# Performance work log

Measured on AMD Instinct MI355X. Metric: run time of the kernel, lower is better.

The kernel has to match this reference:

```python
import jax, jax.numpy as jnp
import numpy as np

N = 50000
D = 128
E = 800000
L = 3


def setup_inputs() -> dict:
    key = jax.random.key(0)
    ks = jax.random.split(key, 6)
    z = jax.random.normal(ks[0], (N, D), dtype=jnp.float32)
    edge_index = jax.random.randint(ks[1], (2, E), 0, N, dtype=jnp.int64)
    s1 = 1.0 / np.sqrt(2 * D)
    s2 = 1.0 / np.sqrt(D)
    # per-layer MLP params, stacked over layers: y = x @ W + b (W stored input-major)
    W1 = jax.random.uniform(ks[2], (L, 2 * D, D), jnp.float32, -s1, s1)
    b1 = jax.random.uniform(ks[3], (L, D), jnp.float32, -s1, s1)
    W2 = jax.random.uniform(ks[4], (L, D, D), jnp.float32, -s2, s2)
    b2 = jax.random.uniform(ks[5], (L, D), jnp.float32, -s2, s2)
    return {"z": z, "edge_index": edge_index, "W1": W1, "b1": b1, "W2": W2, "b2": b2}


def _edgeconv(h, src, dst, W1, b1, W2, b2):
    # message: mlp(cat[x_i, x_j]) per edge; x_i = target (dst), x_j = source (src)
    tmp = jnp.concatenate([h[dst], h[src]], axis=1)           # [E, 2D]
    m = jax.nn.relu(tmp @ W1 + b1) @ W2 + b2                  # [E, D]
    agg = jax.ops.segment_max(m, dst, num_segments=N)          # [N, D], -inf for empty
    return jnp.where(jnp.isfinite(agg), agg, 0.0)


def reference(z, edge_index, W1, b1, W2, b2):
    src = edge_index[0]
    dst = edge_index[1]
    h = z
    for l in range(L - 1):
        h = jax.nn.relu(_edgeconv(h, src, dst, W1[l], b1[l], W2[l], b2[l]))
    h = _edgeconv(h, src, dst, W1[L - 1], b1[L - 1], W2[L - 1], b2[L - 1])
    return h
```

## Files before the change

### kernel.cpp

```cpp
#include <hip/hip_runtime.h>

#define DH 128
#define NLAYER 3
typedef unsigned short ushort_t;
typedef __attribute__((ext_vector_type(8))) short bf16x8;
typedef __attribute__((ext_vector_type(4))) float f32x4;

__device__ __forceinline__ ushort_t f2bf(float a) {
    unsigned u = __float_as_uint(a);
    return (ushort_t)((u + 0x7fffu + ((u >> 16) & 1u)) >> 16);
}
__device__ __forceinline__ float bf2f(ushort_t h) {
    return __uint_as_float(((unsigned)h) << 16);
}
__device__ __forceinline__ unsigned cvtpk(float a, float b) {
    unsigned r;
    asm("v_cvt_pk_bf16_f32 %0, %1, %2" : "=v"(r) : "v"(a), "v"(b));
    return r;
}

__device__ __forceinline__ unsigned enc_f(float f) {
    unsigned u = __float_as_uint(f);
    return (u & 0x80000000u) ? ~u : (u | 0x80000000u);
}
__device__ __forceinline__ float dec_f(unsigned u) {
    unsigned b = (u & 0x80000000u) ? (u ^ 0x80000000u) : ~u;
    return __uint_as_float(b);
}
#define ENC_NEG_INF 0x007FFFFFu

__global__ void fill_u(unsigned* __restrict__ p, int n, unsigned v) {
    int i = blockIdx.x * blockDim.x + threadIdx.x;
    int stride = gridDim.x * blockDim.x;
    for (; i < n; i += stride) p[i] = v;
}

__global__ void hist_kernel(const int* __restrict__ dst, unsigned* __restrict__ cnt, int E) {
    int e = blockIdx.x * blockDim.x + threadIdx.x;
    int stride = gridDim.x * blockDim.x;
    for (; e < E; e += stride) atomicAdd(&cnt[dst[e]], 1u);
}

__global__ __launch_bounds__(1024) void scan_local(const unsigned* __restrict__ cnt,
                                                   unsigned* __restrict__ off,
                                                   unsigned* __restrict__ bsum, int n) {
    __shared__ unsigned s[1024];
    const int t = threadIdx.x;
    int idx = blockIdx.x * 1024 + t;
    unsigned v = (idx < n) ? cnt[idx] : 0u;
    s[t] = v;
    __syncthreads();
    for (int d = 1; d < 1024; d <<= 1) {
        unsigned u = (t >= d) ? s[t - d] : 0u;
        __syncthreads();
        s[t] += u;
        __syncthreads();
    }
    if (idx < n) off[idx] = s[t] - v;
    if (t == 1023) bsum[blockIdx.x] = s[t];
}
__global__ void scan_base(unsigned* __restrict__ bsum, int nb) {
    __shared__ unsigned s[64];
    const int t = threadIdx.x;
    unsigned v = (t < nb) ? bsum[t] : 0u;
    s[t] = v;
    __syncthreads();
    for (int d = 1; d < 64; d <<= 1) {
        unsigned u = (t >= d) ? s[t - d] : 0u;
        __syncthreads();
        s[t] += u;
        __syncthreads();
    }
    if (t < nb) bsum[t] = s[t] - v;
}
__global__ void scan_add(unsigned* __restrict__ off, const unsigned* __restrict__ bsum,
                         unsigned* __restrict__ cnt, int n) {
    int i = blockIdx.x * blockDim.x + threadIdx.x;
    int stride = gridDim.x * blockDim.x;
    for (; i < n; i += stride) { off[i] += bsum[i >> 10]; cnt[i] = 0u; }
}

__global__ void scatter_kernel(const int* __restrict__ src, const int* __restrict__ dst,
                               const unsigned* __restrict__ off, unsigned* __restrict__ cur,
                               int* __restrict__ s_src, int* __restrict__ s_dst, int E) {
    int e = blockIdx.x * blockDim.x + threadIdx.x;
    int stride = gridDim.x * blockDim.x;
    for (; e < E; e += stride) {
        int d = dst[e];
        unsigned p = off[d] + atomicAdd(&cur[d], 1u);
        s_src[p] = src[e];
        s_dst[p] = d;
    }
}

__global__ void convert_w(const float* __restrict__ W1, const float* __restrict__ W2,
                          ushort_t* __restrict__ W1t_hi, ushort_t* __restrict__ W1t_lo,
                          ushort_t* __restrict__ W2t_hi, ushort_t* __restrict__ W2t_lo) {
    const int T1 = NLAYER * 256 * DH, T2 = NLAYER * DH * DH;
    int i = blockIdx.x * blockDim.x + threadIdx.x;
    int stride = gridDim.x * blockDim.x;
    for (; i < T1 + T2; i += stride) {
        if (i < T1) {
            int l = i >> 15, r = i & 32767, c = r >> 7, k = r & 127;
            float w = W1[(size_t)l * 32768 + (size_t)((c < 128) ? k : 128 + k) * DH + (c & 127)];
            ushort_t hi = f2bf(w);
            W1t_hi[i] = hi; W1t_lo[i] = f2bf(w - bf2f(hi));
        } else {
            int j = i - T1;
            int l = j >> 14, r = j & 16383, c = r >> 7, k = r & 127;
            float w = W2[(size_t)l * 16384 + (size_t)k * DH + c];
            ushort_t hi = f2bf(w);
            W2t_hi[j] = hi; W2t_lo[j] = f2bf(w - bf2f(hi));
        }
    }
}

__global__ __launch_bounds__(256, 2) void node_gemm(
    const float* __restrict__ zin, const unsigned* __restrict__ aggin,
    const float* __restrict__ b2prev,
    const ushort_t* __restrict__ wthi, const ushort_t* __restrict__ wtlo,
    const float* __restrict__ b1, float* __restrict__ outA, float* __restrict__ outB,
    int N, int nrb, int mode) {
    __shared__ char smem[33280];
    float* b2s = (float*)(smem + 32768);
    const int t = threadIdx.x;
    const int w = t >> 6, l = t & 63;
    const int bb = blockIdx.x;
    const int half = (bb >= nrb) ? 1 : 0;
    const ushort_t* whi = wthi + (size_t)(half ? 128 : 0) * DH;
    const ushort_t* wlo = wtlo + (size_t)(half ? 128 : 0) * DH;
    float* outp = half ? outB : outA;
    const int n0 = (bb - half * nrb) * 128;

    if (t < 128) b2s[t] = mode ? b2prev[t] : 0.0f;
    #pragma unroll
    for (int i = 0; i < 4; ++i) {
        int cid = i * 256 + t;
        int cc = cid >> 4, ch = cid & 15;
        int sc = ch ^ (cc & 15);
        uint4 vh = *(const uint4*)(whi + (size_t)cc * DH + sc * 8);
        uint4 vl = *(const uint4*)(wlo + (size_t)cc * DH + sc * 8);
        *(uint4*)(smem + cid * 16) = vh;
        *(uint4*)(smem + 16384 + cid * 16) = vl;
    }
    __syncthreads();

    bf16x8 ahi[2][4], alo[2][4];
    #pragma unroll
    for (int rt = 0; rt < 2; ++rt) {
        int row = n0 + w * 32 + rt * 16 + (l & 15);
        if (row >= N) row = N - 1;
        size_t base = (size_t)row * DH + 8 * (l >> 4);
        const int kbase = 8 * (l >> 4);
        #pragma unroll
        for (int ks = 0; ks < 4; ++ks) {
            float v0, v1, v2, v3, v4, v5, v6, v7;
            if (mode == 0) {
                float4 a0 = *(const float4*)(zin + base + ks * 32);
                float4 a1 = *(const float4*)(zin + base + ks * 32 + 4);
                v0 = a0.x; v1 = a0.y; v2 = a0.z; v3 = a0.w;
                v4 = a1.x; v5 = a1.y; v6 = a1.z; v7 = a1.w;
            } else {
                uint4 u0 = *(const uint4*)(aggin + base + ks * 32);
                uint4 u1 = *(const uint4*)(aggin + base + ks * 32 + 4);
                float4 c0 = *(const float4*)&b2s[kbase + ks * 32];
                float4 c1 = *(const float4*)&b2s[kbase + ks * 32 + 4];
                v0 = fmaxf((u0.x == ENC_NEG_INF) ? 0.0f : dec_f(u0.x) + c0.x, 0.0f);
                v1 = fmaxf((u0.y == ENC_NEG_INF) ? 0.0f : dec_f(u0.y) + c0.y, 0.0f);
                v2 = fmaxf((u0.z == ENC_NEG_INF) ? 0.0f : dec_f(u0.z) + c0.z, 0.0f);
                v3 = fmaxf((u0.w == ENC_NEG_INF) ? 0.0f : dec_f(u0.w) + c0.w, 0.0f);
                v4 = fmaxf((u1.x == ENC_NEG_INF) ? 0.0f : dec_f(u1.x) + c1.x, 0.0f);
                v5 = fmaxf((u1.y == ENC_NEG_INF) ? 0.0f : dec_f(u1.y) + c1.y, 0.0f);
                v6 = fmaxf((u1.z == ENC_NEG_INF) ? 0.0f : dec_f(u1.z) + c1.z, 0.0f);
                v7 = fmaxf((u1.w == ENC_NEG_INF) ? 0.0f : dec_f(u1.w) + c1.w, 0.0f);
            }
            unsigned h01 = cvtpk(v0, v1), h23 = cvtpk(v2, v3);
            unsigned h45 = cvtpk(v4, v5), h67 = cvtpk(v6, v7);
            float l0 = v0 - __uint_as_float(h01 << 16);
            float l1 = v1 - __uint_as_float(h01 & 0xffff0000u);
            float l2 = v2 - __uint_as_float(h23 << 16);
            float l3 = v3 - __uint_as_float(h23 & 0xffff0000u);
            float l4 = v4 - __uint_as_float(h45 << 16);
            float l5 = v5 - __uint_as_float(h45 & 0xffff0000u);
            float l6 = v6 - __uint_as_float(h67 << 16);
            float l7 = v7 - __uint_as_float(h67 & 0xffff0000u);
            unsigned q01 = cvtpk(l0, l1), q23 = cvtpk(l2, l3);
            unsigned q45 = cvtpk(l4, l5), q67 = cvtpk(l6, l7);
            uint4 hp = {h01, h23, h45, h67};
            uint4 lp = {q01, q23, q45, q67};
            ahi[rt][ks] = *(bf16x8*)&hp;
            alo[rt][ks] = *(bf16x8*)&lp;
        }
    }
    f32x4 acc[2][8];
    #pragma unroll
    for (int rt = 0; rt < 2; ++rt)
        #pragma unroll
        for (int ct = 0; ct < 8; ++ct) acc[rt][ct] = (f32x4){0.f, 0.f, 0.f, 0.f};
    #pragma unroll
    for (int ct = 0; ct < 4; ++ct) {
        int colv = ct * 16 + (l & 15);
        #pragma unroll
        for (int ks = 0; ks < 4; ++ks) {
            int chb = ks * 4 + (l >> 4);
            int addr = colv * 256 + ((chb ^ (colv & 15)) << 4);
            bf16x8 bh = *(const bf16x8*)(smem + addr);
            bf16x8 bl = *(const bf16x8*)(smem + 16384 + addr);
            #pragma unroll
            for (int rt = 0; rt < 2; ++rt) {
                acc[rt][ct] = __builtin_amdgcn_mfma_f32_16x16x32_bf16(ahi[rt][ks], bh, acc[rt][ct], 0, 0, 0);
                acc[rt][ct] = __builtin_amdgcn_mfma_f32_16x16x32_bf16(ahi[rt][ks], bl, acc[rt][ct], 0, 0, 0);
                acc[rt][ct] = __builtin_amdgcn_mfma_f32_16x16x32_bf16(alo[rt][ks], bh, acc[rt][ct], 0, 0, 0);
            }
        }
    }
    __syncthreads();
    #pragma unroll
    for (int i = 0; i < 4; ++i) {
        int cid = i * 256 + t;
        int cc = cid >> 4, ch = cid & 15;
        int sc = ch ^ (cc & 15);
        uint4 vh = *(const uint4*)(whi + (size_t)(64 + cc) * DH + sc * 8);
        uint4 vl = *(const uint4*)(wlo + (size_t)(64 + cc) * DH + sc * 8);
        *(uint4*)(smem + cid * 16) = vh;
        *(uint4*)(smem + 16384 + cid * 16) = vl;
    }
    __syncthreads();
    #pragma unroll
    for (int ct = 4; ct < 8; ++ct) {
        int colv = ct * 16 + (l & 15);
        #pragma unroll
        for (int ks = 0; ks < 4; ++ks) {
            int chb = ks * 4 + (l >> 4);
            int addr = (colv & 63) * 256 + ((chb ^ (colv & 15)) << 4);
            bf16x8 bh = *(const bf16x8*)(smem + addr);
            bf16x8 bl = *(const bf16x8*)(smem + 16384 + addr);
            #pragma unroll
            for (int rt = 0; rt < 2; ++rt) {
                acc[rt][ct] = __builtin_amdgcn_mfma_f32_16x16x32_bf16(ahi[rt][ks], bh, acc[rt][ct], 0, 0, 0);
                acc[rt][ct] = __builtin_amdgcn_mfma_f32_16x16x32_bf16(ahi[rt][ks], bl, acc[rt][ct], 0, 0, 0);
                acc[rt][ct] = __builtin_amdgcn_mfma_f32_16x16x32_bf16(alo[rt][ks], bh, acc[rt][ct], 0, 0, 0);
            }
        }
    }
    #pragma unroll
    for (int ct = 0; ct < 8; ++ct) {
        int col = ct * 16 + (l & 15);
        float bv = half ? 0.0f : b1[col];
        #pragma unroll
        for (int rt = 0; rt < 2; ++rt)
            #pragma unroll
            for (int i = 0; i < 4; ++i) {
                int row = n0 + w * 32 + rt * 16 + (l >> 4) * 4 + i;
                if (row < N) outp[(size_t)row * DH + col] = acc[rt][ct][i] + bv;
            }
    }
}

__global__ __launch_bounds__(256, 2) void edge_mlp(
    const float* __restrict__ Afp, const float* __restrict__ Bfp,
    const int* __restrict__ src, const int* __restrict__ dst,
    const ushort_t* __restrict__ w2hi, const ushort_t* __restrict__ w2lo,
    unsigned* __restrict__ agg, int E) {
    __shared__ char smem[33280];
    int* sdst = (int*)(smem + 32768);
    float* R = (float*)smem;
    const int t = threadIdx.x;
    const int w = t >> 6, l = t & 63;
    const int e0 = blockIdx.x * 128;

    if (t < 128) sdst[t] = dst[e0 + t];
    #pragma unroll
    for (int i = 0; i < 4; ++i) {
        int cid = i * 256 + t;
        int cc = cid >> 4, ch = cid & 15;
        int sc = ch ^ (cc & 15);
        uint4 vh = *(const uint4*)(w2hi + (size_t)cc * DH + sc * 8);
        uint4 vl = *(const uint4*)(w2lo + (size_t)cc * DH + sc * 8);
        *(uint4*)(smem + cid * 16) = vh;
        *(uint4*)(smem + 16384 + cid * 16) = vl;
    }

    bf16x8 ahi[2][4], alo[2][4];
    #pragma unroll
    for (int rt = 0; rt < 2; ++rt) {
        int er = w * 32 + rt * 16 + (l & 15);
        int dn = dst[e0 + er], sn = src[e0 + er];
        const float* pa = Afp + (size_t)dn * DH + 8 * (l >> 4);
        const float* pb = Bfp + (size_t)sn * DH + 8 * (l >> 4);
        #pragma unroll
        for (int ks = 0; ks < 4; ++ks) {
            float4 a0 = *(const float4*)(pa + ks * 32);
            float4 a1 = *(const float4*)(pa + ks * 32 + 4);
            float4 b0 = *(const float4*)(pb + ks * 32);
            float4 b1 = *(const float4*)(pb + ks * 32 + 4);
            float v0 = fmaxf(a0.x + b0.x, 0.f), v1 = fmaxf(a0.y + b0.y, 0.f);
            float v2 = fmaxf(a0.z + b0.z, 0.f), v3 = fmaxf(a0.w + b0.w, 0.f);
            float v4 = fmaxf(a1.x + b1.x, 0.f), v5 = fmaxf(a1.y + b1.y, 0.f);
            float v6 = fmaxf(a1.z + b1.z, 0.f), v7 = fmaxf(a1.w + b1.w, 0.f);
            unsigned h01 = cvtpk(v0, v1), h23 = cvtpk(v2, v3);
            unsigned h45 = cvtpk(v4, v5), h67 = cvtpk(v6, v7);
            float l0 = v0 - __uint_as_float(h01 << 16);
            float l1 = v1 - __uint_as_float(h01 & 0xffff0000u);
            float l2 = v2 - __uint_as_float(h23 << 16);
            float l3 = v3 - __uint_as_float(h23 & 0xffff0000u);
            float l4 = v4 - __uint_as_float(h45 << 16);
            float l5 = v5 - __uint_as_float(h45 & 0xffff0000u);
            float l6 = v6 - __uint_as_float(h67 << 16);
            float l7 = v7 - __uint_as_float(h67 & 0xffff0000u);
            unsigned q01 = cvtpk(l0, l1), q23 = cvtpk(l2, l3);
            unsigned q45 = cvtpk(l4, l5), q67 = cvtpk(l6, l7);
            uint4 hp = {h01, h23, h45, h67};
            uint4 lp = {q01, q23, q45, q67};
            ahi[rt][ks] = *(bf16x8*)&hp;
            alo[rt][ks] = *(bf16x8*)&lp;
        }
    }
    f32x4 acc[2][8];
    #pragma unroll
    for (int rt = 0; rt < 2; ++rt)
        #pragma unroll
        for (int ct = 0; ct < 8; ++ct) acc[rt][ct] = (f32x4){0.f, 0.f, 0.f, 0.f};
    __syncthreads();
    #pragma unroll
    for (int ct = 0; ct < 4; ++ct) {
        int colv = ct * 16 + (l & 15);
        #pragma unroll
        for (int ks = 0; ks < 4; ++ks) {
            int chb = ks * 4 + (l >> 4);
            int addr = colv * 256 + ((chb ^ (colv & 15)) << 4);
            bf16x8 bh = *(const bf16x8*)(smem + addr);
            bf16x8 bl = *(const bf16x8*)(smem + 16384 + addr);
            #pragma unroll
            for (int rt = 0; rt < 2; ++rt) {
                acc[rt][ct] = __builtin_amdgcn_mfma_f32_16x16x32_bf16(ahi[rt][ks], bh, acc[rt][ct], 0, 0, 0);
                acc[rt][ct] = __builtin_amdgcn_mfma_f32_16x16x32_bf16(ahi[rt][ks], bl, acc[rt][ct], 0, 0, 0);
                acc[rt][ct] = __builtin_amdgcn_mfma_f32_16x16x32_bf16(alo[rt][ks], bh, acc[rt][ct], 0, 0, 0);
            }
        }
    }
    __syncthreads();
    #pragma unroll
    for (int i = 0; i < 4; ++i) {
        int cid = i * 256 + t;
        int cc = cid >> 4, ch = cid & 15;
        int sc = ch ^ (cc & 15);
        uint4 vh = *(const uint4*)(w2hi + (size_t)(64 + cc) * DH + sc * 8);
        uint4 vl = *(const uint4*)(w2lo + (size_t)(64 + cc) * DH + sc * 8);
        *(uint4*)(smem + cid * 16) = vh;
        *(uint4*)(smem + 16384 + cid * 16) = vl;
    }
    __syncthreads();
    #pragma unroll
    for (int ct = 4; ct < 8; ++ct) {
        int colv = ct * 16 + (l & 15);
        #pragma unroll
        for (int ks = 0; ks < 4; ++ks) {
            int chb = ks * 4 + (l >> 4);
            int addr = (colv & 63) * 256 + ((chb ^ (colv & 15)) << 4);
            bf16x8 bh = *(const bf16x8*)(smem + addr);
            bf16x8 bl = *(const bf16x8*)(smem + 16384 + addr);
            #pragma unroll
            for (int rt = 0; rt < 2; ++rt) {
                acc[rt][ct] = __builtin_amdgcn_mfma_f32_16x16x32_bf16(ahi[rt][ks], bh, acc[rt][ct], 0, 0, 0);
                acc[rt][ct] = __builtin_amdgcn_mfma_f32_16x16x32_bf16(ahi[rt][ks], bl, acc[rt][ct], 0, 0, 0);
                acc[rt][ct] = __builtin_amdgcn_mfma_f32_16x16x32_bf16(alo[rt][ks], bh, acc[rt][ct], 0, 0, 0);
            }
        }
    }
    #pragma unroll
    for (int chh = 0; chh < 2; ++chh) {
        __syncthreads();
        #pragma unroll
        for (int rt = 0; rt < 2; ++rt)
            #pragma unroll
            for (int c4 = 0; c4 < 4; ++c4) {
                int ct = chh * 4 + c4;
                int col64 = c4 * 16 + (l & 15);
                #pragma unroll
                for (int i = 0; i < 4; ++i) {
                    int row = w * 32 + rt * 16 + (l >> 4) * 4 + i;
                    R[row * 64 + (col64 ^ (((row >> 2) & 3) << 4))] = acc[rt][ct][i];
                }
            }
        __syncthreads();
        const int col = l;
        const int r0 = w * 32;
        float run = R[r0 * 64 + (col ^ (((r0 >> 2) & 3) << 4))];
        int cur = sdst[r0];
        #pragma unroll
        for (int rr = r0 + 1; rr < r0 + 32; ++rr) {
            float x = R[rr * 64 + (col ^ (((rr >> 2) & 3) << 4))];
            int dd = sdst[rr];
            if (dd != cur) {
                atomicMax(&agg[(size_t)cur * DH + chh * 64 + col], enc_f(run));
                cur = dd; run = x;
            } else {
                run = fmaxf(run, x);
            }
        }
        atomicMax(&agg[(size_t)cur * DH + chh * 64 + col], enc_f(run));
    }
}

__global__ void finalize_kernel(const unsigned* __restrict__ agg, const float* __restrict__ b2,
                                float* __restrict__ outf, int n) {
    int i = blockIdx.x * blockDim.x + threadIdx.x;
    int stride = gridDim.x * blockDim.x;
    for (; i < n; i += stride) {
        unsigned uv = agg[i];
        outf[i] = (uv == ENC_NEG_INF) ? 0.0f : dec_f(uv) + b2[i & (DH - 1)];
    }
}

extern "C" void kernel_launch(void* const* d_in, const int* in_sizes, int n_in,
                              void* d_out, int out_size, void* d_ws, size_t ws_size,
                              hipStream_t stream) {
    const float* z  = (const float*)d_in[0];
    const int*   ei = (const int*)d_in[1];
    const float* W1 = (const float*)d_in[2];
    const float* b1 = (const float*)d_in[3];
    const float* W2 = (const float*)d_in[4];
    const float* b2 = (const float*)d_in[5];
    const int N = 50000, D = DH, E = 800000;
    const int* srcp = ei;
    const int* dstp = ei + E;

    float* Abuf = (float*)d_ws;
    float* Bbuf = Abuf + (size_t)N * D;
    unsigned* agg = (unsigned*)(Bbuf + (size_t)N * D);
    ushort_t* W1t_hi = (ushort_t*)(agg + (size_t)N * D);
    ushort_t* W1t_lo = W1t_hi + NLAYER * 256 * D;
    ushort_t* W2t_hi = W1t_lo + NLAYER * 256 * D;
    ushort_t* W2t_lo = W2t_hi + NLAYER * D * D;
    unsigned* cnt = (unsigned*)(W2t_lo + NLAYER * D * D);
    unsigned* off = cnt + N;
    unsigned* bsum = off + N;
    int* s_src = (int*)(bsum + 64);
    int* s_dst = s_src + E;
    float* outp = (float*)d_out;

    convert_w<<<128, 256, 0, stream>>>(W1, W2, W1t_hi, W1t_lo, W2t_hi, W2t_lo);

    const int NB = (N + 1023) / 1024;
    fill_u<<<256, 256, 0, stream>>>(cnt, N, 0u);
    hist_kernel<<<1024, 256, 0, stream>>>(dstp, cnt, E);
    scan_local<<<NB, 1024, 0, stream>>>(cnt, off, bsum, N);
    scan_base<<<1, 64, 0, stream>>>(bsum, NB);
    scan_add<<<256, 256, 0, stream>>>(off, bsum, cnt, N);
    scatter_kernel<<<1024, 256, 0, stream>>>(srcp, dstp, off, cnt, s_src, s_dst, E);

    const int nrb = (N + 127) / 128;
    for (int l = 0; l < NLAYER; ++l) {
        node_gemm<<<2 * nrb, 256, 0, stream>>>(z, agg,
                                               (l > 0) ? (b2 + (size_t)(l - 1) * D) : nullptr,
                                               W1t_hi + ((size_t)l * 256) * D,
                                               W1t_lo + ((size_t)l * 256) * D,
                                               b1 + (size_t)l * D, Abuf, Bbuf,
                                               N, nrb, (l > 0) ? 1 : 0);
        fill_u<<<2048, 256, 0, stream>>>(agg, N * D, ENC_NEG_INF);
        edge_mlp<<<E / 128, 256, 0, stream>>>(Abuf, Bbuf, s_src, s_dst,
                                              W2t_hi + (size_t)l * D * D,
                                              W2t_lo + (size_t)l * D * D, agg, E);
    }
    finalize_kernel<<<2048, 256, 0, stream>>>(agg, b2 + (size_t)2 * D, outp, N * D);
}
```

Measured before the change: 753.2 us.

## Split edge MLP output columns across 8 waves with full W2 in LDS

The edge_mlp block grows from 256 to 512 threads. Each of the 8 waves now handles 32 edges by 64 output columns instead of 32 edges by all 128 columns. The whole W2 hi/lo split is staged into 64KB of LDS once, which removes the second weight load and its extra barriers. Per-wave LDS slabs replace the shared reduction buffer for the segmented max. The cost is that each edge's A/B gather and bf16 split conversion now run in two waves, and the larger LDS footprint may limit blocks per CU.

```diff
diff --git a/kernel.cpp b/kernel.cpp
--- a/kernel.cpp
+++ b/kernel.cpp
@@ -257,34 +257,35 @@
     }
 }
 
-__global__ __launch_bounds__(256, 2) void edge_mlp(
+__global__ __launch_bounds__(512, 4) void edge_mlp(
     const float* __restrict__ Afp, const float* __restrict__ Bfp,
     const int* __restrict__ src, const int* __restrict__ dst,
     const ushort_t* __restrict__ w2hi, const ushort_t* __restrict__ w2lo,
     unsigned* __restrict__ agg, int E) {
-    __shared__ char smem[33280];
-    int* sdst = (int*)(smem + 32768);
-    float* R = (float*)smem;
+    __shared__ char smem[66048];
+    int* sdst = (int*)(smem + 65536);
     const int t = threadIdx.x;
     const int w = t >> 6, l = t & 63;
     const int e0 = blockIdx.x * 128;
+    const int ew = (w & 3) * 32;
+    const int colbase = (w >> 2) * 64;
 
     if (t < 128) sdst[t] = dst[e0 + t];
     #pragma unroll
     for (int i = 0; i < 4; ++i) {
-        int cid = i * 256 + t;
+        int cid = i * 512 + t;
         int cc = cid >> 4, ch = cid & 15;
         int sc = ch ^ (cc & 15);
         uint4 vh = *(const uint4*)(w2hi + (size_t)cc * DH + sc * 8);
         uint4 vl = *(const uint4*)(w2lo + (size_t)cc * DH + sc * 8);
         *(uint4*)(smem + cid * 16) = vh;
-        *(uint4*)(smem + 16384 + cid * 16) = vl;
+        *(uint4*)(smem + 32768 + cid * 16) = vl;
     }
 
     bf16x8 ahi[2][4], alo[2][4];
     #pragma unroll
     for (int rt = 0; rt < 2; ++rt) {
-        int er = w * 32 + rt * 16 + (l & 15);
+        int er = ew + rt * 16 + (l & 15);
         int dn = dst[e0 + er], sn = src[e0 + er];
         const float* pa = Afp + (size_t)dn * DH + 8 * (l >> 4);
         const float* pb = Bfp + (size_t)sn * DH + 8 * (l >> 4);
@@ -316,21 +317,21 @@
             alo[rt][ks] = *(bf16x8*)&lp;
         }
     }
-    f32x4 acc[2][8];
+    f32x4 acc[2][4];
     #pragma unroll
     for (int rt = 0; rt < 2; ++rt)
         #pragma unroll
-        for (int ct = 0; ct < 8; ++ct) acc[rt][ct] = (f32x4){0.f, 0.f, 0.f, 0.f};
+        for (int ct = 0; ct < 4; ++ct) acc[rt][ct] = (f32x4){0.f, 0.f, 0.f, 0.f};
     __syncthreads();
     #pragma unroll
     for (int ct = 0; ct < 4; ++ct) {
-        int colv = ct * 16 + (l & 15);
+        int colv = colbase + ct * 16 + (l & 15);
         #pragma unroll
         for (int ks = 0; ks < 4; ++ks) {
             int chb = ks * 4 + (l >> 4);
             int addr = colv * 256 + ((chb ^ (colv & 15)) << 4);
             bf16x8 bh = *(const bf16x8*)(smem + addr);
-            bf16x8 bl = *(const bf16x8*)(smem + 16384 + addr);
+            bf16x8 bl = *(const bf16x8*)(smem + 32768 + addr);
             #pragma unroll
             for (int rt = 0; rt < 2; ++rt) {
                 acc[rt][ct] = __builtin_amdgcn_mfma_f32_16x16x32_bf16(ahi[rt][ks], bh, acc[rt][ct], 0, 0, 0);
@@ -340,67 +341,34 @@
         }
     }
     __syncthreads();
-    #pragma unroll
-    for (int i = 0; i < 4; ++i) {
-        int cid = i * 256 + t;
-        int cc = cid >> 4, ch = cid & 15;
-        int sc = ch ^ (cc & 15);
-        uint4 vh = *(const uint4*)(w2hi + (size_t)(64 + cc) * DH + sc * 8);
-        uint4 vl = *(const uint4*)(w2lo + (size_t)(64 + cc) * DH + sc * 8);
-        *(uint4*)(smem + cid * 16) = vh;
-        *(uint4*)(smem + 16384 + cid * 16) = vl;
-    }
-    __syncthreads();
-    #pragma unroll
-    for (int ct = 4; ct < 8; ++ct) {
-        int colv = ct * 16 + (l & 15);
-        #pragma unroll
-        for (int ks = 0; ks < 4; ++ks) {
-            int chb = ks * 4 + (l >> 4);
-            int addr = (colv & 63) * 256 + ((chb ^ (colv & 15)) << 4);
-            bf16x8 bh = *(const bf16x8*)(smem + addr);
-            bf16x8 bl = *(const bf16x8*)(smem + 16384 + addr);
+    float* slab = (float*)(smem + w * 8192);
+    #pragma unroll
+    for (int rt = 0; rt < 2; ++rt)
+        #pragma unroll
+        for (int ct = 0; ct < 4; ++ct) {
+            int col64 = ct * 16 + (l & 15);
             #pragma unroll
-            for (int rt = 0; rt < 2; ++rt) {
-                acc[rt][ct] = __builtin_amdgcn_mfma_f32_16x16x32_bf16(ahi[rt][ks], bh, acc[rt][ct], 0, 0, 0);
-                acc[rt][ct] = __builtin_amdgcn_mfma_f32_16x16x32_bf16(ahi[rt][ks], bl, acc[rt][ct], 0, 0, 0);
-                acc[rt][ct] = __builtin_amdgcn_mfma_f32_16x16x32_bf16(alo[rt][ks], bh, acc[rt][ct], 0, 0, 0);
-            }
-        }
-    }
-    #pragma unroll
-    for (int chh = 0; chh < 2; ++chh) {
-        __syncthreads();
-        #pragma unroll
-        for (int rt = 0; rt < 2; ++rt)
-            #pragma unroll
-            for (int c4 = 0; c4 < 4; ++c4) {
-                int ct = chh * 4 + c4;
-                int col64 = c4 * 16 + (l & 15);
-                #pragma unroll
-                for (int i = 0; i < 4; ++i) {
-                    int row = w * 32 + rt * 16 + (l >> 4) * 4 + i;
-                    R[row * 64 + (col64 ^ (((row >> 2) & 3) << 4))] = acc[rt][ct][i];
-                }
-            }
-        __syncthreads();
-        const int col = l;
-        const int r0 = w * 32;
-        float run = R[r0 * 64 + (col ^ (((r0 >> 2) & 3) << 4))];
-        int cur = sdst[r0];
-        #pragma unroll
-        for (int rr = r0 + 1; rr < r0 + 32; ++rr) {
-            float x = R[rr * 64 + (col ^ (((rr >> 2) & 3) << 4))];
-            int dd = sdst[rr];
-            if (dd != cur) {
-                atomicMax(&agg[(size_t)cur * DH + chh * 64 + col], enc_f(run));
-                cur = dd; run = x;
-            } else {
-                run = fmaxf(run, x);
-            }
-        }
-        atomicMax(&agg[(size_t)cur * DH + chh * 64 + col], enc_f(run));
-    }
+            for (int i = 0; i < 4; ++i) {
+                int row = rt * 16 + (l >> 4) * 4 + i;
+                slab[row * 64 + (col64 ^ (((row >> 2) & 3) << 4))] = acc[rt][ct][i];
+            }
+        }
+    __syncthreads();
+    const int col = l;
+    float run = slab[(col ^ 0)];
+    int cur = sdst[ew];
+    #pragma unroll
+    for (int rr = 1; rr < 32; ++rr) {
+        float x = slab[rr * 64 + (col ^ (((rr >> 2) & 3) << 4))];
+        int dd = sdst[ew + rr];
+        if (dd != cur) {
+            atomicMax(&agg[(size_t)cur * DH + colbase + col], enc_f(run));
+            cur = dd; run = x;
+        } else {
+            run = fmaxf(run, x);
+        }
+    }
+    atomicMax(&agg[(size_t)cur * DH + colbase + col], enc_f(run));
 }
 
 __global__ void finalize_kernel(const unsigned* __restrict__ agg, const float* __restrict__ b2,
@@ -459,7 +427,7 @@
                                                b1 + (size_t)l * D, Abuf, Bbuf,
                                                N, nrb, (l > 0) ? 1 : 0);
         fill_u<<<2048, 256, 0, stream>>>(agg, N * D, ENC_NEG_INF);
-        edge_mlp<<<E / 128, 256, 0, stream>>>(Abuf, Bbuf, s_src, s_dst,
+        edge_mlp<<<E / 128, 512, 0, stream>>>(Abuf, Bbuf, s_src, s_dst,
                                               W2t_hi + (size_t)l * D * D,
                                               W2t_lo + (size_t)l * D * D, agg, E);
     }
```

Result: no change. 748.4 us (-0.6%).

## Stage unique destination rows in shared memory before edge MLP gather

Applied to the files above, without the earlier changes.

Each block runs a prefix scan over its 128 destination indices to find distinct runs, then loads up to 32 unique destination feature rows into shared memory once. Edges then read their target-side operand from LDS instead of gathering it again from global memory, with a global fallback when a block has more than 32 unique destinations. This only pays off if edges arrive sorted by destination. With random edge order almost every block has about 128 unique destinations, so the scan's many barriers and the extra 16KB of LDS, which may reduce occupancy, become overhead.

```diff
diff --git a/kernel.cpp b/kernel.cpp
--- a/kernel.cpp
+++ b/kernel.cpp
@@ -262,8 +262,12 @@
     const int* __restrict__ src, const int* __restrict__ dst,
     const ushort_t* __restrict__ w2hi, const ushort_t* __restrict__ w2lo,
     unsigned* __restrict__ agg, int E) {
-    __shared__ char smem[33280];
-    int* sdst = (int*)(smem + 32768);
+    __shared__ char smem[50432];
+    float (*Ash)[DH] = (float (*)[DH])(smem + 32768);
+    int* sdst = (int*)(smem + 49152);
+    int* sscan = (int*)(smem + 49664);
+    int* rowhead = (int*)(smem + 50176);
+    int* nuni = (int*)(smem + 50304);
     float* R = (float*)smem;
     const int t = threadIdx.x;
     const int w = t >> 6, l = t & 63;
@@ -280,14 +284,43 @@
         *(uint4*)(smem + cid * 16) = vh;
         *(uint4*)(smem + 16384 + cid * 16) = vl;
     }
+    __syncthreads();
+    if (t < 128) sscan[t] = (t == 0 || sdst[t] != sdst[t - 1]) ? 1 : 0;
+    __syncthreads();
+    for (int d = 1; d < 128; d <<= 1) {
+        int v = 0;
+        if (t < 128 && t >= d) v = sscan[t - d];
+        __syncthreads();
+        if (t < 128) sscan[t] += v;
+        __syncthreads();
+    }
+    if (t < 128) {
+        int nf = (t == 0 || sdst[t] != sdst[t - 1]);
+        int sl = sscan[t] - 1;
+        if (nf && sl < 32) rowhead[sl] = sdst[t];
+        if (t == 127) *nuni = sscan[127];
+    }
+    __syncthreads();
+    {
+        int nu = *nuni; if (nu > 32) nu = 32;
+        for (int i = t; i < nu * 32; i += 256) {
+            int slot = i >> 5, ch = i & 31;
+            *(float4*)&Ash[slot][ch * 4] =
+                *(const float4*)&Afp[(size_t)rowhead[slot] * DH + ch * 4];
+        }
+    }
+    __syncthreads();
 
     bf16x8 ahi[2][4], alo[2][4];
     #pragma unroll
     for (int rt = 0; rt < 2; ++rt) {
         int er = w * 32 + rt * 16 + (l & 15);
-        int dn = dst[e0 + er], sn = src[e0 + er];
-        const float* pa = Afp + (size_t)dn * DH + 8 * (l >> 4);
+        int slot = sscan[er] - 1;
+        int sn = src[e0 + er];
         const float* pb = Bfp + (size_t)sn * DH + 8 * (l >> 4);
+        const float* pa;
+        if (slot < 32) pa = &Ash[slot][8 * (l >> 4)];
+        else           pa = Afp + (size_t)sdst[er] * DH + 8 * (l >> 4);
         #pragma unroll
         for (int ks = 0; ks < 4; ++ks) {
             float4 a0 = *(const float4*)(pa + ks * 32);
@@ -321,7 +354,6 @@
     for (int rt = 0; rt < 2; ++rt)
         #pragma unroll
         for (int ct = 0; ct < 8; ++ct) acc[rt][ct] = (f32x4){0.f, 0.f, 0.f, 0.f};
-    __syncthreads();
     #pragma unroll
     for (int ct = 0; ct < 4; ++ct) {
         int colv = ct * 16 + (l & 15);
```

Result: no change. 767.6 us (+1.9%).
